# Performance work log

Measured on AMD Instinct MI355X. Metric: run time of the kernel, lower is better.

## Reference

```python
import jax, jax.numpy as jnp
import numpy as np

B, L, IN, H, W = 4096, 10, 8, 512, 512


def setup_inputs() -> dict:
    key = jax.random.key(0)
    ks = jax.random.split(key, 24)
    s = 0.05  # small init so tanh/sigmoid stay in active range
    def rn(k, shape):
        return jax.random.normal(k, shape, dtype=jnp.float32) * s
    return {
        "items": jax.random.normal(ks[0], (B, L, IN), dtype=jnp.float32),
        "decoder_items_input": jax.random.uniform(ks[1], (B, H), dtype=jnp.float32),
        "emb_w": rn(ks[2], (H, IN)), "emb_b": rn(ks[3], (H,)),
        "enc_wih": rn(ks[4], (3 * H, H)), "enc_whh": rn(ks[5], (3 * H, H)),
        "enc_bih": rn(ks[6], (3 * H,)), "enc_bhh": rn(ks[7], (3 * H,)),
        "dec_wih": rn(ks[8], (3 * H, H)), "dec_whh": rn(ks[9], (3 * H, H)),
        "dec_bih": rn(ks[10], (3 * H,)), "dec_bhh": rn(ks[11], (3 * H,)),
        "w1": rn(ks[12], (W, H)), "w2": rn(ks[13], (W, H)),
        "w3": rn(ks[14], (W, H)), "w4": rn(ks[15], (W, H)),
        "w5": rn(ks[16], (W, H)), "w6": rn(ks[17], (W, H)),
        "w7": rn(ks[18], (W, 2 * H)),
        "v1": rn(ks[19], (W,)), "v2": rn(ks[20], (W,)),
        "v3_w": rn(ks[21], (W,)), "v3_b": rn(ks[22], (1,)),
        "wori": rn(ks[23], (6, 3 * H)), "bori": jnp.zeros((6,), jnp.float32),
    }


def _gru_scan(xg, whh, bhh, h0):
    # xg: [L,B,3H] precomputed input-gate projections; returns all hidden states [L,B,H]
    def step(h, xg_t):
        hg = h @ whh.T + bhh
        xr, xz, xn = jnp.split(xg_t, 3, axis=-1)
        hr, hz, hn = jnp.split(hg, 3, axis=-1)
        r = jax.nn.sigmoid(xr + hr)
        z = jax.nn.sigmoid(xz + hz)
        n = jnp.tanh(xn + r * hn)
        h_new = (1.0 - z) * n + z * h
        return h_new, h_new
    _, ys = jax.lax.scan(step, h0, xg)
    return ys


def _forward(items, decoder_items_input, emb_w, emb_b, enc_wih, enc_whh, enc_bih, enc_bhh,
             dec_wih, dec_whh, dec_bih, dec_bhh, w1, w2, w3, w4, w5, w6, w7,
             v1, v2, v3_w, v3_b, wori, bori):
    Bsz, Lln, _ = items.shape
    Hh = emb_w.shape[0]
    x = items @ emb_w.T + emb_b                                  # [B,L,H] embedding
    xg = (x @ enc_wih.T + enc_bih).transpose(1, 0, 2)            # [L,B,3H]
    enc_out = _gru_scan(xg, enc_whh, enc_bhh, jnp.zeros((Bsz, Hh), x.dtype))  # [L,B,H]
    h0 = enc_out[-1]                                             # last encoder state
    enc_blh = enc_out.transpose(1, 0, 2)                         # [B,L,H]
    enc_w3 = enc_out @ w3.T                                      # [L,B,W] (hoisted, step-invariant)
    enc_w6 = enc_out @ w6.T                                      # [L,B,W]
    xg_dec = decoder_items_input @ dec_wih.T + dec_bih           # [B,3H] constant decoder input
    xr, xz, xn = jnp.split(xg_dec, 3, axis=-1)

    def step(h, _):
        hg = h @ dec_whh.T + dec_bhh
        hr, hz, hn = jnp.split(hg, 3, axis=-1)
        r = jax.nn.sigmoid(xr + hr)
        z = jax.nn.sigmoid(xz + hz)
        n = jnp.tanh(xn + r * hn)
        h_new = (1.0 - z) * n + z * h                            # GRUCell update
        # intra attention cache is always length-1 in the source (the shape[1]==1 branch
        # always fires), so log_softmax is over a singleton axis -> exactly zero.
        doi = h_new[:, None, :]                                  # [B,1,H]
        oi = jnp.tanh(h_new @ w1.T + h_new @ w2.T) @ v1          # [B]
        attnd = jax.nn.log_softmax(oi[:, None, None], axis=-1)   # [B,1,1] zeros
        hi = (attnd * doi).sum(axis=1)                           # [B,H] (zeros, faithful)
        sm = jnp.tanh(enc_w3 + h_new @ w4.T + hi @ w5.T)         # [L,B,W]
        out_seq = (sm @ v2).T                                    # [B,L]
        sm_ori = jnp.tanh(enc_w6 + jnp.concatenate([h_new, hi], axis=-1) @ w7.T)  # [L,B,W]
        oo = sm_ori @ v3_w + v3_b[0]                             # [L,B]
        attnc = jax.nn.log_softmax(oo.T[:, :, None], axis=-1)    # [B,L,1] zeros (singleton axis)
        he = (attnc * enc_blh).sum(axis=1)                       # [B,H]
        total = jnp.concatenate([he, h_new, hi], axis=-1)        # [B,3H]
        out_ori = total @ wori.T + bori                          # [B,6]
        return h_new, (out_seq, out_ori)

    _, (seqs, oris) = jax.lax.scan(step, h0, None, length=Lln)
    probs_seq = seqs.transpose(1, 0, 2)                          # [B,L,L]
    probs_ori = oris.transpose(1, 0, 2)                          # [B,L,6]
    return probs_seq, probs_ori


def reference(items, decoder_items_input, emb_w, emb_b, enc_wih, enc_whh, enc_bih, enc_bhh,
              dec_wih, dec_whh, dec_bih, dec_bhh, w1, w2, w3, w4, w5, w6, w7,
              v1, v2, v3_w, v3_b, wori, bori):
    return _forward(items, decoder_items_input, emb_w, emb_b, enc_wih, enc_whh, enc_bih,
                    enc_bhh, dec_wih, dec_whh, dec_bih, dec_bhh, w1, w2, w3, w4, w5, w6,
                    w7, v1, v2, v3_w, v3_b, wori, bori)
```

## Files before the change

kernel.cpp:

```cpp
#include <hip/hip_runtime.h>
#include <hip/hip_bf16.h>


#define B_   4096
#define L_   10
#define IN_  8
#define H_   512
#define H3_  1536
#define W_   512
#define ORI_BASE (B_ * L_ * L_)

typedef __attribute__((ext_vector_type(8))) short s8v;
typedef __attribute__((ext_vector_type(4))) short s4v;
typedef __attribute__((ext_vector_type(4))) float f4v;

#define LOG2E  1.4426950408889634f
#define LOG2E2 2.8853900817779268f

__device__ __forceinline__ float sig_fast(float x) {
  float e = __builtin_amdgcn_exp2f(-x * LOG2E);
  return __builtin_amdgcn_rcpf(1.f + e);
}
__device__ __forceinline__ float tanh_fast(float x) {
  float e = __builtin_amdgcn_exp2f(x * LOG2E2);
  return 1.f - 2.f * __builtin_amdgcn_rcpf(e + 1.f);
}
__device__ __forceinline__ short f2bf(float f) {
  __hip_bfloat16 h = __float2bfloat16(f);
  return __builtin_bit_cast(short, h);
}
__device__ __forceinline__ float bf2f(short s) {
  __hip_bfloat16 h = __builtin_bit_cast(__hip_bfloat16, s);
  return __bfloat162float(h);
}
__device__ __forceinline__ void stc(float* p, float v) { *p = v; }
__device__ __forceinline__ void stc(short* p, float v) { *p = f2bf(v); }

__global__ __launch_bounds__(256) void prep_all(
    const float* __restrict__ s0, short* __restrict__ d0,
    const float* __restrict__ s1, short* __restrict__ d1,
    const float* __restrict__ s2, short* __restrict__ d2,
    const float* __restrict__ s3, short* __restrict__ d3,
    const float* __restrict__ s4, short* __restrict__ d4,
    const float* __restrict__ s5, short* __restrict__ d5)
{
  long i8 = (long)blockIdx.x * 256 + threadIdx.x;
  const float* s; short* d; long off;
  if      (i8 < 98304)  { s = s0; d = d0; off = i8; }
  else if (i8 < 196608) { s = s1; d = d1; off = i8 - 98304; }
  else if (i8 < 294912) { s = s2; d = d2; off = i8 - 196608; }
  else if (i8 < 327680) { s = s3; d = d3; off = i8 - 294912; }
  else if (i8 < 360448) { s = s4; d = d4; off = i8 - 327680; }
  else if (i8 < 622592) { s = s5; d = d5; off = i8 - 360448; }
  else return;
  const float* sp = s + off * 8;
  s8v v;
#pragma unroll
  for (int j = 0; j < 8; ++j) v[j] = f2bf(sp[j]);
  *(s8v*)(d + off * 8) = v;
}

__global__ __launch_bounds__(256) void build_wc(
    const float* __restrict__ enc_wih, const float* __restrict__ emb_w,
    const float* __restrict__ emb_b, const float* __restrict__ enc_bih,
    float* __restrict__ Wc, float* __restrict__ bc)
{
  __shared__ float se[H_ * IN_];
  __shared__ float sb[H_];
  const int tid = threadIdx.x;
  for (int i = tid; i < H_ * IN_; i += 256) se[i] = emb_w[i];
  for (int i = tid; i < H_; i += 256) sb[i] = emb_b[i];
  __syncthreads();
  int g = (blockIdx.x * 256 + tid) >> 6;
  int lane = tid & 63;
  const float* wr = enc_wih + (long)g * H_ + lane * 8;
  float w8[8];
#pragma unroll
  for (int j = 0; j < 8; ++j) w8[j] = wr[j];
  float acc[9] = {};
#pragma unroll
  for (int kk = 0; kk < 8; ++kk) {
    int k = lane * 8 + kk;
#pragma unroll
    for (int j = 0; j < 8; ++j) acc[j] += w8[kk] * se[k * IN_ + j];
    acc[8] += w8[kk] * sb[k];
  }
#pragma unroll
  for (int j = 0; j < 9; ++j)
#pragma unroll
    for (int off = 32; off; off >>= 1) acc[j] += __shfl_down(acc[j], off, 64);
  if (lane == 0) {
#pragma unroll
    for (int j = 0; j < 8; ++j) Wc[g * IN_ + j] = acc[j];
    bc[g] = acc[8] + enc_bih[g];
  }
}

template <typename CT>
__global__ __launch_bounds__(256) void gemm_bf16(
    const short* __restrict__ A, long lda,
    const short* __restrict__ Bw, long ldb,
    const float* __restrict__ bias,
    CT* __restrict__ C, long ldc, int K, float scale)
{
  __shared__ short As[2][128 * 64];
  __shared__ short Bs[2][128 * 64];
  const int tid = threadIdx.x;
  const long row0 = (long)blockIdx.y * 128;
  const long col0 = (long)blockIdx.x * 128;
  const int wave = tid >> 6, lane = tid & 63;
  const int wm = (wave & 1) * 64, wn = (wave >> 1) * 64;
  const int r16 = lane & 15, quad = lane >> 4;
  const int sw = r16 & 7;
  f4v acc[4][4] = {};

  auto stage = [&](int buf, int k0) {
#pragma unroll
    for (int r = 0; r < 4; ++r) {
      int idx = r * 256 + tid;
      int m = idx >> 3, c8 = idx & 7;
      int src = c8 ^ (m & 7);
      __builtin_amdgcn_global_load_lds(
          (const __attribute__((address_space(1))) void*)(A + (row0 + m) * lda + k0 + src * 8),
          (__attribute__((address_space(3))) void*)(&As[buf][idx * 8]), 16, 0, 0);
    }
#pragma unroll
    for (int r = 0; r < 4; ++r) {
      int idx = r * 256 + tid;
      int m = idx >> 3, c8 = idx & 7;
      int src = c8 ^ (m & 7);
      __builtin_amdgcn_global_load_lds(
          (const __attribute__((address_space(1))) void*)(Bw + (col0 + m) * ldb + k0 + src * 8),
          (__attribute__((address_space(3))) void*)(&Bs[buf][idx * 8]), 16, 0, 0);
    }
  };

  const int nk = K >> 6;
  stage(0, 0);
  for (int k = 0; k < nk; ++k) {
    if (k < nk - 1) {
      stage((k + 1) & 1, (k + 1) * 64);
      asm volatile("s_waitcnt vmcnt(8)" ::: "memory");
    } else {
      asm volatile("s_waitcnt vmcnt(0)" ::: "memory");
    }
    __builtin_amdgcn_s_barrier();
    const short* Asc = As[k & 1];
    const short* Bsc = Bs[k & 1];
    s8v af[4][2], bf[4][2];
#pragma unroll
    for (int i = 0; i < 4; ++i)
#pragma unroll
      for (int hh = 0; hh < 2; ++hh)
        af[i][hh] = *(const s8v*)&Asc[(wm + i * 16 + r16) * 64 + ((hh * 4 + quad) ^ sw) * 8];
#pragma unroll
    for (int j = 0; j < 4; ++j)
#pragma unroll
      for (int hh = 0; hh < 2; ++hh)
        bf[j][hh] = *(const s8v*)&Bsc[(wn + j * 16 + r16) * 64 + ((hh * 4 + quad) ^ sw) * 8];
    __builtin_amdgcn_s_setprio(1);
#pragma unroll
    for (int hh = 0; hh < 2; ++hh)
#pragma unroll
      for (int i = 0; i < 4; ++i)
#pragma unroll
        for (int j = 0; j < 4; ++j)
          acc[i][j] = __builtin_amdgcn_mfma_f32_16x16x32_bf16(af[i][hh], bf[j][hh], acc[i][j], 0, 0, 0);
    __builtin_amdgcn_s_setprio(0);
    __builtin_amdgcn_s_barrier();
  }

#pragma unroll
  for (int i = 0; i < 4; ++i) {
    long rbase = row0 + wm + i * 16 + quad * 4;
#pragma unroll
    for (int j = 0; j < 4; ++j) {
      long c = col0 + wn + j * 16 + r16;
      float bv = bias ? bias[c] : 0.f;
#pragma unroll
      for (int rg = 0; rg < 4; ++rg)
        stc(&C[(rbase + rg) * ldc + c], (acc[i][j][rg] + bv) * scale);
    }
  }
}

template <bool ENC>
__global__ __launch_bounds__(256) void gru_fused(
    const short* __restrict__ Aprev,
    const short* __restrict__ Whh,
    const float* __restrict__ bhh,
    const short* __restrict__ xg,
    const float* __restrict__ items_t,
    const float* __restrict__ Wc,
    const float* __restrict__ bc,
    float* __restrict__ h,
    short* __restrict__ hout)
{
  __shared__ short As[2][64 * 64];
  __shared__ short Bs[2][192 * 64];
  const int tid = threadIdx.x;
  const long row0 = (long)blockIdx.y * 64;
  const int col0 = blockIdx.x * 64;
  const int wave = tid >> 6, lane = tid & 63;
  const int r16 = lane & 15, quad = lane >> 4;
  const int sw = r16 & 7;

  f4v acc[3][4] = {};

  auto stage = [&](int buf, int k0) {
#pragma unroll
    for (int r = 0; r < 2; ++r) {
      int idx = r * 256 + tid;
      int m = idx >> 3, c8 = idx & 7;
      int src = c8 ^ (m & 7);
      __builtin_amdgcn_global_load_lds(
          (const __attribute__((address_space(1))) void*)(Aprev + (row0 + m) * H_ + k0 + src * 8),
          (__attribute__((address_space(3))) void*)(&As[buf][idx * 8]), 16, 0, 0);
    }
#pragma unroll
    for (int r = 0; r < 6; ++r) {
      int idx = r * 256 + tid;
      int m = idx >> 3, c8 = idx & 7;
      int src = c8 ^ (m & 7);
      int g = m >> 6, cc = m & 63;
      __builtin_amdgcn_global_load_lds(
          (const __attribute__((address_space(1))) void*)(Whh + ((long)g * H_ + col0 + cc) * H_ + k0 + src * 8),
          (__attribute__((address_space(3))) void*)(&Bs[buf][idx * 8]), 16, 0, 0);
    }
  };

  stage(0, 0);
  int cur = 0;
  for (int k = 0; k < 8; ++k) {
    if (k < 7) {
      stage(cur ^ 1, (k + 1) * 64);
      asm volatile("s_waitcnt vmcnt(8)" ::: "memory");
    } else {
      asm volatile("s_waitcnt vmcnt(0)" ::: "memory");
    }
    __builtin_amdgcn_s_barrier();
    s8v af[4][2], bf[3][2];
#pragma unroll
    for (int i = 0; i < 4; ++i)
#pragma unroll
      for (int hh = 0; hh < 2; ++hh)
        af[i][hh] = *(const s8v*)&As[cur][(i * 16 + r16) * 64 + ((hh * 4 + quad) ^ sw) * 8];
#pragma unroll
    for (int g = 0; g < 3; ++g)
#pragma unroll
      for (int hh = 0; hh < 2; ++hh)
        bf[g][hh] = *(const s8v*)&Bs[cur][(g * 64 + wave * 16 + r16) * 64 + ((hh * 4 + quad) ^ sw) * 8];
    __builtin_amdgcn_s_setprio(1);
#pragma unroll
    for (int hh = 0; hh < 2; ++hh)
#pragma unroll
      for (int g = 0; g < 3; ++g)
#pragma unroll
        for (int i = 0; i < 4; ++i)
          acc[g][i] = __builtin_amdgcn_mfma_f32_16x16x32_bf16(af[i][hh], bf[g][hh], acc[g][i], 0, 0, 0);
    __builtin_amdgcn_s_setprio(0);
    __builtin_amdgcn_s_barrier();
    cur ^= 1;
  }

  const int col = col0 + wave * 16 + r16;
  float wc[3][8], bcv[3];
  if (ENC) {
#pragma unroll
    for (int g = 0; g < 3; ++g) {
      const float* wr = Wc + ((long)g * H_ + col) * IN_;
#pragma unroll
      for (int j = 0; j < 8; ++j) wc[g][j] = wr[j];
      bcv[g] = bc[g * H_ + col];
    }
    float* itemS = (float*)As;
    int i2 = tid * 2;
    int m = i2 >> 3, j = i2 & 7;
    itemS[i2] = items_t[(row0 + m) * (L_ * IN_) + j];
    itemS[i2 + 1] = items_t[(row0 + m) * (L_ * IN_) + j + 1];
    __syncthreads();
  }
  float bhr = bhh[col], bhz = bhh[col + H_], bhn = bhh[col + 2 * H_];

#pragma unroll
  for (int i = 0; i < 4; ++i) {
#pragma unroll
    for (int rg = 0; rg < 4; ++rg) {
      int rl = i * 16 + quad * 4 + rg;
      long row = row0 + rl;
      float xr, xz, xn;
      if (ENC) {
        const float* it = (const float*)As + rl * 8;
        xr = bcv[0]; xz = bcv[1]; xn = bcv[2];
#pragma unroll
        for (int j = 0; j < 8; ++j) {
          float iv = it[j];
          xr += iv * wc[0][j];
          xz += iv * wc[1][j];
          xn += iv * wc[2][j];
        }
      } else {
        long gx = row * H3_ + col;
        xr = bf2f(xg[gx]); xz = bf2f(xg[gx + H_]); xn = bf2f(xg[gx + 2 * H_]);
      }
      float r = sig_fast(xr + acc[0][i][rg] + bhr);
      float z = sig_fast(xz + acc[1][i][rg] + bhz);
      float n = tanh_fast(xn + r * (acc[2][i][rg] + bhn));
      long hi = row * H_ + col;
      float hv = (1.f - z) * n + z * h[hi];
      h[hi] = hv;
      hout[hi] = f2bf(hv);
    }
  }
}

__global__ __launch_bounds__(256) void out_seq_all(
    const short* __restrict__ ew3,
    const short* __restrict__ a4,
    const float* __restrict__ v2,
    float* __restrict__ out)
{
  __shared__ float se[L_ * W_];
  __shared__ float sa[L_ * W_];
  const int b = blockIdx.x;
  const int tid = threadIdx.x;
  for (int i = tid; i < L_ * 128; i += 256) {
    int row = i >> 7, q = i & 127;
    s4v ev = *(const s4v*)(ew3 + ((long)row * B_ + b) * W_ + q * 4);
    s4v av = *(const s4v*)(a4 + ((long)row * B_ + b) * W_ + q * 4);
    f4v e, a;
#pragma unroll
    for (int j = 0; j < 4; ++j) { e[j] = bf2f(ev[j]); a[j] = bf2f(av[j]); }
    *(f4v*)(se + row * W_ + q * 4) = e;
    *(f4v*)(sa + row * W_ + q * 4) = a;
  }
  const int wave = tid >> 6, lane = tid & 63;
  float sv0[4], sv1[4], svtot = 0.f;
#pragma unroll
  for (int q = 0; q < 4; ++q) {
    float v = v2[lane * 4 + q];
    sv0[q] = -2.f * v; svtot += v;
    v = v2[256 + lane * 4 + q];
    sv1[q] = -2.f * v; svtot += v;
  }
#pragma unroll
  for (int off = 32; off; off >>= 1) svtot += __shfl_down(svtot, off, 64);
  svtot = __shfl(svtot, 0, 64);
  __syncthreads();

  int tprev = -1;
  f4v a0, a1;
#pragma unroll
  for (int pp = 0; pp < 25; ++pp) {
    int p = wave * 25 + pp;
    int t = p / L_, l = p - t * L_;
    if (t != tprev) {
      a0 = *(const f4v*)(sa + t * W_ + lane * 4);
      a1 = *(const f4v*)(sa + t * W_ + 256 + lane * 4);
      tprev = t;
    }
    f4v e0 = *(const f4v*)(se + l * W_ + lane * 4);
    f4v e1 = *(const f4v*)(se + l * W_ + 256 + lane * 4);
    float acc = 0.f;
#pragma unroll
    for (int q = 0; q < 4; ++q) {
      float x0 = __builtin_amdgcn_exp2f(e0[q] + a0[q]);
      acc += sv0[q] * __builtin_amdgcn_rcpf(x0 + 1.f);
      float x1 = __builtin_amdgcn_exp2f(e1[q] + a1[q]);
      acc += sv1[q] * __builtin_amdgcn_rcpf(x1 + 1.f);
    }
#pragma unroll
    for (int off = 32; off; off >>= 1) acc += __shfl_down(acc, off, 64);
    if (lane == 0) out[((long)b * L_ + t) * L_ + l] = svtot + acc;
  }
}

__global__ __launch_bounds__(256) void out_ori_all(
    const short* __restrict__ dh,
    const float* __restrict__ wori, const float* __restrict__ bori,
    float* __restrict__ out)
{
  int wid = (blockIdx.x * 256 + threadIdx.x) >> 6;
  int lane = threadIdx.x & 63;
  int b = wid / L_, t = wid - b * L_;
  s8v hv = *(const s8v*)(dh + ((long)t * B_ + b) * H_ + lane * 8);
  float hf[8];
#pragma unroll
  for (int j = 0; j < 8; ++j) hf[j] = bf2f(hv[j]);
  float res[6];
#pragma unroll
  for (int o = 0; o < 6; ++o) {
    const float* wr = wori + (long)o * H3_ + H_ + lane * 8;
    float acc = 0.f;
#pragma unroll
    for (int j = 0; j < 8; ++j) acc += hf[j] * wr[j];
#pragma unroll
    for (int off = 32; off; off >>= 1) acc += __shfl_down(acc, off, 64);
    res[o] = acc;
  }
  if (lane == 0) {
    float* po = out + ORI_BASE + ((long)b * L_ + t) * 6;
#pragma unroll
    for (int o = 0; o < 6; ++o) po[o] = res[o] + bori[o];
  }
}

extern "C" void kernel_launch(void* const* d_in, const int* in_sizes, int n_in,
                              void* d_out, int out_size, void* d_ws, size_t ws_size,
                              hipStream_t stream)
{
  const float* items   = (const float*)d_in[0];
  const float* dec_in  = (const float*)d_in[1];
  const float* emb_w   = (const float*)d_in[2];
  const float* emb_b   = (const float*)d_in[3];
  const float* enc_wih = (const float*)d_in[4];
  const float* enc_whh = (const float*)d_in[5];
  const float* enc_bih = (const float*)d_in[6];
  const float* enc_bhh = (const float*)d_in[7];
  const float* dec_wih = (const float*)d_in[8];
  const float* dec_whh = (const float*)d_in[9];
  const float* dec_bih = (const float*)d_in[10];
  const float* dec_bhh = (const float*)d_in[11];
  const float* w3      = (const float*)d_in[14];
  const float* w4      = (const float*)d_in[15];
  const float* v2      = (const float*)d_in[20];
  const float* wori    = (const float*)d_in[23];
  const float* bori    = (const float*)d_in[24];
  float* out = (float*)d_out;

  char* ws = (char*)d_ws;
  size_t off = 0;
  auto alloc = [&](size_t bytes) { size_t o = off; off += (bytes + 255) & ~255UL; return o; };
  float* Wc       = (float*)(ws + alloc(H3_ * IN_ * 4));
  float* bc       = (float*)(ws + alloc(H3_ * 4));
  float* h        = (float*)(ws + alloc((size_t)B_ * H_ * 4));
  short* xgb      = (short*)(ws + alloc((size_t)B_ * H3_ * 2));
  short* enc_hist = (short*)(ws + alloc((size_t)11 * B_ * H_ * 2));
  short* dec_hist = (short*)(ws + alloc((size_t)L_ * B_ * H_ * 2));
  short* ew3      = (short*)(ws + alloc((size_t)L_ * B_ * W_ * 2));
  short* a4       = (short*)(ws + alloc((size_t)L_ * B_ * W_ * 2));
  short* whh_e    = (short*)(ws + alloc((size_t)H3_ * H_ * 2));
  short* whh_d    = (short*)(ws + alloc((size_t)H3_ * H_ * 2));
  short* wih_d    = (short*)(ws + alloc((size_t)H3_ * H_ * 2));
  short* w3b      = (short*)(ws + alloc((size_t)W_ * H_ * 2));
  short* w4b      = (short*)(ws + alloc((size_t)W_ * H_ * 2));
  short* decb     = (short*)(ws + alloc((size_t)B_ * H_ * 2));

  prep_all<<<(622592 + 255) / 256, 256, 0, stream>>>(
      enc_whh, whh_e, dec_whh, whh_d, dec_wih, wih_d,
      w3, w3b, w4, w4b, dec_in, decb);
  build_wc<<<384, 256, 0, stream>>>(enc_wih, emb_w, emb_b, enc_bih, Wc, bc);

  hipMemsetAsync(h, 0, (size_t)B_ * H_ * 4, stream);
  hipMemsetAsync(enc_hist, 0, (size_t)B_ * H_ * 2, stream);

  gemm_bf16<short><<<dim3(12, 32), 256, 0, stream>>>(
      decb, H_, wih_d, H_, dec_bih, xgb, H3_, H_, 1.f);

  for (int t = 0; t < L_; ++t) {
    gru_fused<true><<<dim3(8, 64), 256, 0, stream>>>(
        enc_hist + (size_t)t * B_ * H_, whh_e, enc_bhh, nullptr,
        items + (size_t)t * IN_, Wc, bc, h,
        enc_hist + (size_t)(t + 1) * B_ * H_);
  }

  for (int t = 0; t < L_; ++t) {
    const short* prev = (t == 0) ? enc_hist + (size_t)10 * B_ * H_
                                 : dec_hist + (size_t)(t - 1) * B_ * H_;
    gru_fused<false><<<dim3(8, 64), 256, 0, stream>>>(
        prev, whh_d, dec_bhh, xgb, nullptr, nullptr, nullptr, h,
        dec_hist + (size_t)t * B_ * H_);
  }

  gemm_bf16<short><<<dim3(4, 320), 256, 0, stream>>>(
      enc_hist + (size_t)B_ * H_, H_, w3b, H_, nullptr, ew3, W_, H_, LOG2E2);
  gemm_bf16<short><<<dim3(4, 320), 256, 0, stream>>>(
      dec_hist, H_, w4b, H_, nullptr, a4, W_, H_, LOG2E2);
  out_seq_all<<<B_, 256, 0, stream>>>(ew3, a4, v2, out);
  out_ori_all<<<(B_ * L_) / 4, 256, 0, stream>>>(dec_hist, wori, bori, out);
}
```

Before: 602.5 us.

## Enlarge GRU tile, load Whh fragments to registers, drop fp32 hidden state

The GRU step kernel now runs 512 threads per block over a 128x64 output tile, so each block reuses its weight columns across twice as many batch rows. It uses a 1D grid with a swizzled block-to-tile mapping, intended to improve L2 locality. Whh fragments are loaded straight from global memory into double-buffered registers instead of staged through LDS, which cuts shared-memory traffic and footprint. The separate fp32 hidden-state buffer is removed: the previous state is read back from the bf16 history. This saves an fp32 read and write per step, but the recurrent state is now carried in bf16 precision.

Result: slower. 687.2 us (+14.1%).

```diff
diff --git a/kernel.cpp b/kernel.cpp
--- a/kernel.cpp
+++ b/kernel.cpp
@@ -185,7 +185,7 @@
 }
 
 template <bool ENC>
-__global__ __launch_bounds__(256) void gru_fused(
+__global__ __launch_bounds__(512) void gru_fused(
     const short* __restrict__ Aprev,
     const short* __restrict__ Whh,
     const float* __restrict__ bhh,
@@ -193,63 +193,66 @@
     const float* __restrict__ items_t,
     const float* __restrict__ Wc,
     const float* __restrict__ bc,
-    float* __restrict__ h,
     short* __restrict__ hout)
 {
-  __shared__ short As[2][64 * 64];
-  __shared__ short Bs[2][192 * 64];
+  __shared__ short As[2][128 * 64];
   const int tid = threadIdx.x;
-  const long row0 = (long)blockIdx.y * 64;
-  const int col0 = blockIdx.x * 64;
-  const int wave = tid >> 6, lane = tid & 63;
+  const int f = blockIdx.x;
+  const int x = f & 7, jj = f >> 3;
+  const int bx = 4 * (x >> 2) + (jj & 3);
+  const int by = 8 * (x & 3) + (jj >> 2);
+  const long row0 = (long)by * 128;
+  const int col0 = bx * 64;
+  const int wv = tid >> 6, lane = tid & 63;
+  const int rw = wv >> 2, cw = wv & 3;
   const int r16 = lane & 15, quad = lane >> 4;
   const int sw = r16 & 7;
+  const int col = col0 + cw * 16 + r16;
 
   f4v acc[3][4] = {};
-
-  auto stage = [&](int buf, int k0) {
+  s8v bfr[2][3][2];
+
+  auto stageA = [&](int buf, int k0) {
 #pragma unroll
     for (int r = 0; r < 2; ++r) {
-      int idx = r * 256 + tid;
+      int idx = r * 512 + tid;
       int m = idx >> 3, c8 = idx & 7;
       int src = c8 ^ (m & 7);
       __builtin_amdgcn_global_load_lds(
           (const __attribute__((address_space(1))) void*)(Aprev + (row0 + m) * H_ + k0 + src * 8),
           (__attribute__((address_space(3))) void*)(&As[buf][idx * 8]), 16, 0, 0);
     }
-#pragma unroll
-    for (int r = 0; r < 6; ++r) {
-      int idx = r * 256 + tid;
-      int m = idx >> 3, c8 = idx & 7;
-      int src = c8 ^ (m & 7);
-      int g = m >> 6, cc = m & 63;
-      __builtin_amdgcn_global_load_lds(
-          (const __attribute__((address_space(1))) void*)(Whh + ((long)g * H_ + col0 + cc) * H_ + k0 + src * 8),
-          (__attribute__((address_space(3))) void*)(&Bs[buf][idx * 8]), 16, 0, 0);
-    }
   };
-
-  stage(0, 0);
-  int cur = 0;
+  const short* wp0 = Whh + ((long)(0 * H_ + col)) * H_ + quad * 8;
+  const short* wp1 = Whh + ((long)(1 * H_ + col)) * H_ + quad * 8;
+  const short* wp2 = Whh + ((long)(2 * H_ + col)) * H_ + quad * 8;
+  auto loadB = [&](int buf, int k0) {
+#pragma unroll
+    for (int hh = 0; hh < 2; ++hh) {
+      bfr[buf][0][hh] = *(const s8v*)(wp0 + k0 + hh * 32);
+      bfr[buf][1][hh] = *(const s8v*)(wp1 + k0 + hh * 32);
+      bfr[buf][2][hh] = *(const s8v*)(wp2 + k0 + hh * 32);
+    }
+  };
+
+  stageA(0, 0);
+  loadB(0, 0);
+#pragma unroll
   for (int k = 0; k < 8; ++k) {
     if (k < 7) {
-      stage(cur ^ 1, (k + 1) * 64);
+      stageA((k + 1) & 1, (k + 1) * 64);
+      loadB((k + 1) & 1, (k + 1) * 64);
       asm volatile("s_waitcnt vmcnt(8)" ::: "memory");
     } else {
       asm volatile("s_waitcnt vmcnt(0)" ::: "memory");
     }
     __builtin_amdgcn_s_barrier();
-    s8v af[4][2], bf[3][2];
+    s8v af[4][2];
 #pragma unroll
     for (int i = 0; i < 4; ++i)
 #pragma unroll
       for (int hh = 0; hh < 2; ++hh)
-        af[i][hh] = *(const s8v*)&As[cur][(i * 16 + r16) * 64 + ((hh * 4 + quad) ^ sw) * 8];
-#pragma unroll
-    for (int g = 0; g < 3; ++g)
-#pragma unroll
-      for (int hh = 0; hh < 2; ++hh)
-        bf[g][hh] = *(const s8v*)&Bs[cur][(g * 64 + wave * 16 + r16) * 64 + ((hh * 4 + quad) ^ sw) * 8];
+        af[i][hh] = *(const s8v*)&As[k & 1][(rw * 64 + i * 16 + r16) * 64 + ((hh * 4 + quad) ^ sw) * 8];
     __builtin_amdgcn_s_setprio(1);
 #pragma unroll
     for (int hh = 0; hh < 2; ++hh)
@@ -257,13 +260,11 @@
       for (int g = 0; g < 3; ++g)
 #pragma unroll
         for (int i = 0; i < 4; ++i)
-          acc[g][i] = __builtin_amdgcn_mfma_f32_16x16x32_bf16(af[i][hh], bf[g][hh], acc[g][i], 0, 0, 0);
+          acc[g][i] = __builtin_amdgcn_mfma_f32_16x16x32_bf16(af[i][hh], bfr[k & 1][g][hh], acc[g][i], 0, 0, 0);
     __builtin_amdgcn_s_setprio(0);
     __builtin_amdgcn_s_barrier();
-    cur ^= 1;
-  }
-
-  const int col = col0 + wave * 16 + r16;
+  }
+
   float wc[3][8], bcv[3];
   if (ENC) {
 #pragma unroll
@@ -286,7 +287,7 @@
   for (int i = 0; i < 4; ++i) {
 #pragma unroll
     for (int rg = 0; rg < 4; ++rg) {
-      int rl = i * 16 + quad * 4 + rg;
+      int rl = rw * 64 + i * 16 + quad * 4 + rg;
       long row = row0 + rl;
       float xr, xz, xn;
       if (ENC) {
@@ -307,8 +308,8 @@
       float z = sig_fast(xz + acc[1][i][rg] + bhz);
       float n = tanh_fast(xn + r * (acc[2][i][rg] + bhn));
       long hi = row * H_ + col;
-      float hv = (1.f - z) * n + z * h[hi];
-      h[hi] = hv;
+      float hp = bf2f(Aprev[hi]);
+      float hv = (1.f - z) * n + z * hp;
       hout[hi] = f2bf(hv);
     }
   }
@@ -433,7 +434,6 @@
   auto alloc = [&](size_t bytes) { size_t o = off; off += (bytes + 255) & ~255UL; return o; };
   float* Wc       = (float*)(ws + alloc(H3_ * IN_ * 4));
   float* bc       = (float*)(ws + alloc(H3_ * 4));
-  float* h        = (float*)(ws + alloc((size_t)B_ * H_ * 4));
   short* xgb      = (short*)(ws + alloc((size_t)B_ * H3_ * 2));
   short* enc_hist = (short*)(ws + alloc((size_t)11 * B_ * H_ * 2));
   short* dec_hist = (short*)(ws + alloc((size_t)L_ * B_ * H_ * 2));
@@ -451,24 +451,23 @@
       w3, w3b, w4, w4b, dec_in, decb);
   build_wc<<<384, 256, 0, stream>>>(enc_wih, emb_w, emb_b, enc_bih, Wc, bc);
 
-  hipMemsetAsync(h, 0, (size_t)B_ * H_ * 4, stream);
   hipMemsetAsync(enc_hist, 0, (size_t)B_ * H_ * 2, stream);
 
   gemm_bf16<short><<<dim3(12, 32), 256, 0, stream>>>(
       decb, H_, wih_d, H_, dec_bih, xgb, H3_, H_, 1.f);
 
   for (int t = 0; t < L_; ++t) {
-    gru_fused<true><<<dim3(8, 64), 256, 0, stream>>>(
+    gru_fused<true><<<256, 512, 0, stream>>>(
         enc_hist + (size_t)t * B_ * H_, whh_e, enc_bhh, nullptr,
-        items + (size_t)t * IN_, Wc, bc, h,
+        items + (size_t)t * IN_, Wc, bc,
         enc_hist + (size_t)(t + 1) * B_ * H_);
   }
 
   for (int t = 0; t < L_; ++t) {
     const short* prev = (t == 0) ? enc_hist + (size_t)10 * B_ * H_
                                  : dec_hist + (size_t)(t - 1) * B_ * H_;
-    gru_fused<false><<<dim3(8, 64), 256, 0, stream>>>(
-        prev, whh_d, dec_bhh, xgb, nullptr, nullptr, nullptr, h,
+    gru_fused<false><<<256, 512, 0, stream>>>(
+        prev, whh_d, dec_bhh, xgb, nullptr, nullptr, nullptr,
         dec_hist + (size_t)t * B_ * H_);
   }
 
```
